# Kernel tuning notes

Measured on AMD Instinct MI355X. Metric: run time of the kernel, lower is better.

## Reference

```python
import jax, jax.numpy as jnp
import numpy as np

MARGIN = 0.3

def setup_inputs() -> dict:
    key = jax.random.key(0)
    k1, k2 = jax.random.split(key)
    embeddings = jax.random.normal(k1, (8192, 512), dtype=jnp.float32)
    labels = jax.random.randint(k2, (8192,), 0, 128, dtype=jnp.int64)
    return {"embeddings": embeddings, "labels": labels}

def _pairwise_euclidean(x):
    # ||xi - xj|| via GEMM, matching torch reference (relu clamp + sqrt(.+1e-16))
    dot = x @ x.T                      # [B, B]
    sq = jnp.diagonal(dot)             # [B]
    d2 = sq[None, :] - 2.0 * dot + sq[:, None]
    d2 = jnp.maximum(d2, 0.0)
    return jnp.sqrt(d2 + 1e-16)

def reference(embeddings, labels):
    n = embeddings.shape[0]
    d = _pairwise_euclidean(embeddings)                 # [B, B]
    same = labels[:, None] == labels[None, :]           # [B, B]
    eye = jnp.eye(n, dtype=bool)
    mask_pos = same & ~eye
    mask_neg = ~same
    # fused masked row-wise reductions (hard mining)
    hardest_pos = jnp.max(jnp.where(mask_pos, d, -jnp.inf), axis=1)  # [B]
    hardest_neg = jnp.min(jnp.where(mask_neg, d, jnp.inf), axis=1)   # [B]
    valid = mask_pos.any(axis=1) & mask_neg.any(axis=1)              # [B]
    per_row = jax.nn.relu(hardest_pos - hardest_neg + MARGIN)
    per_row = jnp.where(valid, per_row, 0.0)
    denom = jnp.maximum(jnp.sum(valid.astype(per_row.dtype)), 1.0)
    return jnp.sum(per_row) / denom
```

## Files before the change

kernel.cpp:

```cpp
#include <hip/hip_runtime.h>

#define BATCH 8192
#define DIM   512
#define NTILE 1152

typedef __attribute__((ext_vector_type(4))) float  f32x4;
typedef __attribute__((ext_vector_type(8))) __bf16 bf16x8;

__device__ __forceinline__ unsigned short f2bf(float x) {
  unsigned u = __float_as_uint(x);
  u = (u + 0x7FFFu + ((u >> 16) & 1u)) >> 16;
  return (unsigned short)u;
}

__device__ __forceinline__ void load_lds16(const void* g, void* l) {
  __builtin_amdgcn_global_load_lds(
      (__attribute__((address_space(1))) void*)(g),
      (__attribute__((address_space(3))) void*)(l), 16, 0, 0);
}

__device__ __forceinline__ unsigned enc(float f) {
  unsigned u = __float_as_uint(f);
  return u ^ (unsigned)(((int)u >> 31) | 0x80000000);
}
__device__ __forceinline__ float dec(unsigned k) {
  unsigned u = (k & 0x80000000u) ? (k ^ 0x80000000u) : ~k;
  return __uint_as_float(u);
}

__global__ __launch_bounds__(256) void prep_kernel(
    const float* __restrict__ X, unsigned short* __restrict__ Xb,
    float* __restrict__ sq, unsigned* __restrict__ ctrl,
    uint4* __restrict__ pos4, uint4* __restrict__ neg4) {
  int gid = blockIdx.x * 256 + threadIdx.x;
  if (gid == 0) {
    ((float*)ctrl)[0] = 0.f;
    ((float*)ctrl)[1] = 0.f;
    ctrl[2] = 0u;
    ctrl[3] = 0u;
  }
  if (gid < 196608) {
    pos4[gid] = (uint4){0u, 0u, 0u, 0u};
    neg4[gid] = (uint4){~0u, ~0u, ~0u, ~0u};
  }
  int wave = threadIdx.x >> 6, lane = threadIdx.x & 63;
  int row = blockIdx.x * 4 + wave;
  const float4* xr = (const float4*)(X + (size_t)row * DIM);
  float4 a = xr[lane * 2];
  float4 b = xr[lane * 2 + 1];
  float s = a.x*a.x + a.y*a.y + a.z*a.z + a.w*a.w
          + b.x*b.x + b.y*b.y + b.z*b.z + b.w*b.w;
  uint4 p;
  p.x = (unsigned)f2bf(a.x) | ((unsigned)f2bf(a.y) << 16);
  p.y = (unsigned)f2bf(a.z) | ((unsigned)f2bf(a.w) << 16);
  p.z = (unsigned)f2bf(b.x) | ((unsigned)f2bf(b.y) << 16);
  p.w = (unsigned)f2bf(b.z) | ((unsigned)f2bf(b.w) << 16);
  ((uint4*)(Xb + (size_t)row * DIM))[lane] = p;
  #pragma unroll
  for (int off = 32; off > 0; off >>= 1) s += __shfl_down(s, off);
  if (lane == 0) sq[row] = s;
}

template<int NI>
__device__ __forceinline__ void gemm_tile(
    const unsigned short* __restrict__ Xb, int i0, int jw,
    unsigned short* Asm, unsigned short* Bsm,
    int wave, int wm, int wn, int quad, int lc, int rc, int gcol,
    f32x4 (&acc)[4][8]) {
  for (int k0 = 0; k0 < DIM; k0 += 64) {
    #pragma unroll
    for (int tt = 0; tt < 4; tt++) {
      int c = wave * 4 + tt;
      int row = c * 8 + rc;
      load_lds16(Xb + (size_t)(i0 + row) * DIM + k0 + gcol, &Asm[c * 512]);
    }
    #pragma unroll
    for (int tt = 0; tt < NI; tt++) {
      int c = wave * NI + tt;
      int row = c * 8 + rc;
      load_lds16(Xb + (size_t)(jw + row) * DIM + k0 + gcol, &Bsm[c * 512]);
    }
    __syncthreads();
    #pragma unroll
    for (int kk = 0; kk < 64; kk += 32) {
      int kc = kk >> 3;
      int asel = ((kc + quad) ^ (lc & 7)) * 8;
      bf16x8 af[4], bfr[NI];
      #pragma unroll
      for (int mi = 0; mi < 4; mi++)
        af[mi] = *(const bf16x8*)&Asm[(wm * 64 + mi * 16 + lc) * 64 + asel];
      #pragma unroll
      for (int ni = 0; ni < NI; ni++)
        bfr[ni] = *(const bf16x8*)&Bsm[(wn * (NI * 16) + ni * 16 + lc) * 64 + asel];
      #pragma unroll
      for (int mi = 0; mi < 4; mi++)
        #pragma unroll
        for (int ni = 0; ni < NI; ni++)
          acc[mi][ni] = __builtin_amdgcn_mfma_f32_16x16x32_bf16(
              af[mi], bfr[ni], acc[mi][ni], 0, 0, 0);
    }
    __syncthreads();
  }
}

template<bool STRAD, int NI, int WNS>
__device__ __forceinline__ void epilogue(
    const f32x4 (&acc)[4][8], const float* __restrict__ sq,
    const int* __restrict__ labels,
    int i0, int jwin, int wm, int wn, int quad, int lc,
    unsigned (*ibuf)[128][2], unsigned (*jbuf)[256][2]) {
  float sqj_r[NI]; int labj_r[NI];
  #pragma unroll
  for (int ni = 0; ni < NI; ni++) {
    int j = jwin + wn * WNS + ni * 16 + lc;
    sqj_r[ni] = sq[j]; labj_r[ni] = labels[j];
  }
  float rpos[16], rneg[16];
  float jp[NI], jn[NI];
  #pragma unroll
  for (int x = 0; x < NI; x++) { jp[x] = -3e38f; jn[x] = 3e38f; }
  #pragma unroll
  for (int mi = 0; mi < 4; mi++) {
    #pragma unroll
    for (int r = 0; r < 4; r++) {
      int ig = i0 + wm * 64 + mi * 16 + quad * 4 + r;
      int li = labels[ig];
      float si = sq[ig];
      float rp = -3e38f, rn = 3e38f;
      #pragma unroll
      for (int ni = 0; ni < NI; ni++) {
        float a = acc[mi][ni][r];
        float v = fmaf(-2.f, a, sqj_r[ni]);
        bool same = (li == labj_r[ni]);
        bool posok = same;
        if (STRAD) posok = same && ((jwin + wn * WNS + ni * 16 + lc) != ig);
        rp = fmaxf(rp, posok ? v : -3e38f);
        rn = fminf(rn, same ? 3e38f : v);
        if (!STRAD) {
          float v2 = fmaf(-2.f, a, si);
          jp[ni] = fmaxf(jp[ni], same ? v2 : -3e38f);
          jn[ni] = fminf(jn[ni], same ? 3e38f : v2);
        }
      }
      rpos[mi * 4 + r] = rp; rneg[mi * 4 + r] = rn;
    }
  }
  #pragma unroll
  for (int m = 1; m <= 8; m <<= 1)
    #pragma unroll
    for (int x = 0; x < 16; x++) {
      rpos[x] = fmaxf(rpos[x], __shfl_xor(rpos[x], m));
      rneg[x] = fminf(rneg[x], __shfl_xor(rneg[x], m));
    }
  if (lc == 0) {
    #pragma unroll
    for (int mi = 0; mi < 4; mi++)
      #pragma unroll
      for (int r = 0; r < 4; r++) {
        int row = wm * 64 + mi * 16 + quad * 4 + r;
        ibuf[wn][row][0] = enc(rpos[mi * 4 + r]);
        ibuf[wn][row][1] = enc(rneg[mi * 4 + r]);
      }
  }
  if (!STRAD) {
    #pragma unroll
    for (int m = 16; m <= 32; m <<= 1)
      #pragma unroll
      for (int x = 0; x < NI; x++) {
        jp[x] = fmaxf(jp[x], __shfl_xor(jp[x], m));
        jn[x] = fminf(jn[x], __shfl_xor(jn[x], m));
      }
    if (quad == 0) {
      #pragma unroll
      for (int ni = 0; ni < NI; ni++) {
        int col = wn * WNS + ni * 16 + lc;
        jbuf[wm][col][0] = enc(jp[ni]);
        jbuf[wm][col][1] = enc(jn[ni]);
      }
    }
  }
}

__global__ __launch_bounds__(256, 2) void triplet_mfma(
    const unsigned short* __restrict__ Xb, const float* __restrict__ sq,
    const int* __restrict__ labels, unsigned* __restrict__ ctrl,
    unsigned* __restrict__ pos_i, unsigned* __restrict__ neg_i,
    unsigned* __restrict__ pos_j, unsigned* __restrict__ neg_j) {
  __shared__ __align__(16) unsigned short Asm[128 * 64];
  __shared__ __align__(16) unsigned short Bsm[256 * 64];
  __shared__ int tshare;

  unsigned (*ibuf)[128][2] = reinterpret_cast<unsigned (*)[128][2]>(&Asm[0]);
  unsigned (*jbuf)[256][2] = reinterpret_cast<unsigned (*)[256][2]>(&Asm[1024]);

  int tid = threadIdx.x;
  int wave = tid >> 6, lane = tid & 63;
  int wm = wave >> 1, wn = wave & 1;
  int quad = lane >> 4, lc = lane & 15;
  int rc = lane >> 3;
  int gcol = ((lane & 7) ^ rc) * 8;

  for (;;) {
    if (tid == 0) tshare = (int)atomicAdd(&ctrl[3], 1u);
    __syncthreads();
    int t = tshare;
    if (t >= NTILE) break;

    int It = 0, Js = 0, q = -1; bool strad = false;
    if (t < 64) { It = t; Js = t >> 1; strad = true; }
    else {
      int u;
      if (t < 1024) u = t - 64;
      else { q = (t - 1024) & 3; u = 960 + ((t - 1024) >> 2); }
      for (int s = 0; s < 64; s++) {
        int c = 31 - (s >> 1);
        if (u < c) { It = s; Js = (s >> 1) + 1 + u; break; }
        u -= c;
      }
    }
    int i0 = It * 128;
    int jw = Js * 256 + (q >= 0 ? q * 64 : 0);

    f32x4 acc[4][8];
    #pragma unroll
    for (int mi = 0; mi < 4; mi++)
      #pragma unroll
      for (int ni = 0; ni < 8; ni++)
        acc[mi][ni] = (f32x4){0.f, 0.f, 0.f, 0.f};

    if (q >= 0) {
      gemm_tile<2>(Xb, i0, jw, Asm, Bsm, wave, wm, wn, quad, lc, rc, gcol, acc);
      epilogue<false, 2, 32>(acc, sq, labels, i0, jw, wm, wn, quad, lc, ibuf, jbuf);
    } else {
      gemm_tile<8>(Xb, i0, jw, Asm, Bsm, wave, wm, wn, quad, lc, rc, gcol, acc);
      if (strad)
        epilogue<true, 8, 128>(acc, sq, labels, i0, jw, wm, wn, quad, lc, ibuf, jbuf);
      else
        epilogue<false, 8, 128>(acc, sq, labels, i0, jw, wm, wn, quad, lc, ibuf, jbuf);
    }
    __syncthreads();

    if (q >= 0) {
      if (tid < 128) {
        unsigned p = max(ibuf[0][tid][0], ibuf[1][tid][0]);
        unsigned n = min(ibuf[0][tid][1], ibuf[1][tid][1]);
        atomicMax(&pos_i[(size_t)Js * BATCH + i0 + tid], p);
        atomicMin(&neg_i[(size_t)Js * BATCH + i0 + tid], n);
      }
      if (tid < 64) {
        unsigned p = max(jbuf[0][tid][0], jbuf[1][tid][0]);
        unsigned n = min(jbuf[0][tid][1], jbuf[1][tid][1]);
        pos_j[(size_t)It * BATCH + jw + tid] = p;
        neg_j[(size_t)It * BATCH + jw + tid] = n;
      }
    } else {
      if (tid < 128) {
        unsigned p = max(ibuf[0][tid][0], ibuf[1][tid][0]);
        unsigned n = min(ibuf[0][tid][1], ibuf[1][tid][1]);
        pos_i[(size_t)Js * BATCH + i0 + tid] = p;
        neg_i[(size_t)Js * BATCH + i0 + tid] = n;
      }
      if (!strad) {
        unsigned p = max(jbuf[0][tid][0], jbuf[1][tid][0]);
        unsigned n = min(jbuf[0][tid][1], jbuf[1][tid][1]);
        pos_j[(size_t)It * BATCH + jw + tid] = p;
        neg_j[(size_t)It * BATCH + jw + tid] = n;
      }
    }
    __syncthreads();
  }
}

__global__ __launch_bounds__(256) void final_kernel(
    const unsigned* __restrict__ pos_i, const unsigned* __restrict__ neg_i,
    const unsigned* __restrict__ pos_j, const unsigned* __restrict__ neg_j,
    const float* __restrict__ sq, unsigned* __restrict__ ctrl,
    float* __restrict__ out) {
  int i = blockIdx.x * 256 + threadIdx.x;
  unsigned pe = 0u, ne = 0xFFFFFFFFu;
  #pragma unroll 4
  for (int s = 0; s < 32; s++) {
    pe = max(pe, pos_i[(size_t)s * BATCH + i]);
    ne = min(ne, neg_i[(size_t)s * BATCH + i]);
  }
  #pragma unroll 4
  for (int s = 0; s < 64; s++) {
    pe = max(pe, pos_j[(size_t)s * BATCH + i]);
    ne = min(ne, neg_j[(size_t)s * BATCH + i]);
  }
  float p = dec(pe), n = dec(ne);
  float term = 0.f, cnt = 0.f;
  if (p > -1e37f && n < 1e37f) {
    float si = sq[i];
    float dp = sqrtf(fmaxf(si + p, 0.f) + 1e-16f);
    float dn = sqrtf(fmaxf(si + n, 0.f) + 1e-16f);
    term = fmaxf(dp - dn + 0.3f, 0.f);
    cnt = 1.f;
  }
  #pragma unroll
  for (int off = 32; off > 0; off >>= 1) {
    term += __shfl_down(term, off);
    cnt  += __shfl_down(cnt, off);
  }
  __shared__ float ss[4], sc[4];
  int wave = threadIdx.x >> 6, lane = threadIdx.x & 63;
  if (lane == 0) { ss[wave] = term; sc[wave] = cnt; }
  __syncthreads();
  if (threadIdx.x == 0) {
    atomicAdd((float*)&ctrl[0], ss[0] + ss[1] + ss[2] + ss[3]);
    atomicAdd((float*)&ctrl[1], sc[0] + sc[1] + sc[2] + sc[3]);
    __threadfence();
    unsigned t = atomicAdd(&ctrl[2], 1u);
    if (t == 31u) {
      float S = atomicAdd((float*)&ctrl[0], 0.f);
      float C = atomicAdd((float*)&ctrl[1], 0.f);
      out[0] = S / fmaxf(C, 1.f);
    }
  }
}

extern "C" void kernel_launch(void* const* d_in, const int* in_sizes, int n_in,
                              void* d_out, int out_size, void* d_ws, size_t ws_size,
                              hipStream_t stream) {
  const float* X      = (const float*)d_in[0];
  const int*   labels = (const int*)d_in[1];
  float* out = (float*)d_out;
  char* ws = (char*)d_ws;

  const size_t SLOT = (size_t)BATCH * 4;
  unsigned short* Xb = (unsigned short*)ws;
  float* sq      = (float*)(ws + (8u << 20));
  unsigned* ctrl = (unsigned*)(ws + (8u << 20) + (32u << 10));
  char*  posb = ws + (8u << 20) + (64u << 10);
  char*  negb = posb + 96 * SLOT;
  unsigned* pos_i = (unsigned*)posb;
  unsigned* pos_j = (unsigned*)(posb + 32 * SLOT);
  unsigned* neg_i = (unsigned*)negb;
  unsigned* neg_j = (unsigned*)(negb + 32 * SLOT);

  prep_kernel<<<BATCH / 4, 256, 0, stream>>>(X, Xb, sq, ctrl,
                                             (uint4*)posb, (uint4*)negb);
  triplet_mfma<<<512, 256, 0, stream>>>(Xb, sq, labels, ctrl,
                                        pos_i, neg_i, pos_j, neg_j);
  final_kernel<<<BATCH / 256, 256, 0, stream>>>(pos_i, neg_i, pos_j, neg_j, sq, ctrl, out);
}
```

Before: 135.4 us.

## Prefetch next tile's first K-slab during epilogue; split final reduction across waves

The persistent GEMM loop now grabs the next tile index before the epilogue and issues the global-to-LDS loads for that tile's first K slab, so they overlap the current tile's epilogue and atomic writes. To make this safe, the epilogue scratch buffers get their own shared memory instead of aliasing the A tile, and one barrier per K loop and one per tile are dropped. The final reduction kernel is relaunched with 128 blocks, each splitting the 96 slot reads across four waves, to raise parallelism for the memory-bound merge. The cost is more shared memory per block, which could limit occupancy, plus extra control-flow complexity.

```diff
diff --git a/kernel.cpp b/kernel.cpp
--- a/kernel.cpp
+++ b/kernel.cpp
@@ -3,6 +3,7 @@
 #define BATCH 8192
 #define DIM   512
 #define NTILE 1152
+#define NFIN  128
 
 typedef __attribute__((ext_vector_type(4))) float  f32x4;
 typedef __attribute__((ext_vector_type(8))) __bf16 bf16x8;
@@ -61,25 +62,45 @@
   if (lane == 0) sq[row] = s;
 }
 
+__device__ __forceinline__ void decode_tile(int t, int& It, int& Js, int& q, bool& strad) {
+  It = 0; Js = 0; q = -1; strad = false;
+  if (t < 64) { It = t; Js = t >> 1; strad = true; return; }
+  int u;
+  if (t < 1024) u = t - 64;
+  else { q = (t - 1024) & 3; u = 960 + ((t - 1024) >> 2); }
+  for (int s = 0; s < 64; s++) {
+    int c = 31 - (s >> 1);
+    if (u < c) { It = s; Js = (s >> 1) + 1 + u; return; }
+    u -= c;
+  }
+}
+
 template<int NI>
-__device__ __forceinline__ void gemm_tile(
+__device__ __forceinline__ void stage_slab(
+    const unsigned short* __restrict__ Xb, int i0, int jw, int k0,
+    unsigned short* Asm, unsigned short* Bsm, int wave, int rc, int gcol) {
+  #pragma unroll
+  for (int tt = 0; tt < 4; tt++) {
+    int c = wave * 4 + tt;
+    int row = c * 8 + rc;
+    load_lds16(Xb + (size_t)(i0 + row) * DIM + k0 + gcol, &Asm[c * 512]);
+  }
+  #pragma unroll
+  for (int tt = 0; tt < NI; tt++) {
+    int c = wave * NI + tt;
+    int row = c * 8 + rc;
+    load_lds16(Xb + (size_t)(jw + row) * DIM + k0 + gcol, &Bsm[c * 512]);
+  }
+}
+
+template<int NI>
+__device__ __forceinline__ void gemm_pf(
     const unsigned short* __restrict__ Xb, int i0, int jw,
     unsigned short* Asm, unsigned short* Bsm,
     int wave, int wm, int wn, int quad, int lc, int rc, int gcol,
     f32x4 (&acc)[4][8]) {
   for (int k0 = 0; k0 < DIM; k0 += 64) {
-    #pragma unroll
-    for (int tt = 0; tt < 4; tt++) {
-      int c = wave * 4 + tt;
-      int row = c * 8 + rc;
-      load_lds16(Xb + (size_t)(i0 + row) * DIM + k0 + gcol, &Asm[c * 512]);
-    }
-    #pragma unroll
-    for (int tt = 0; tt < NI; tt++) {
-      int c = wave * NI + tt;
-      int row = c * 8 + rc;
-      load_lds16(Xb + (size_t)(jw + row) * DIM + k0 + gcol, &Bsm[c * 512]);
-    }
+    if (k0) stage_slab<NI>(Xb, i0, jw, k0, Asm, Bsm, wave, rc, gcol);
     __syncthreads();
     #pragma unroll
     for (int kk = 0; kk < 64; kk += 32) {
@@ -99,7 +120,7 @@
           acc[mi][ni] = __builtin_amdgcn_mfma_f32_16x16x32_bf16(
               af[mi], bfr[ni], acc[mi][ni], 0, 0, 0);
     }
-    __syncthreads();
+    if (k0 < DIM - 64) __syncthreads();
   }
 }
 
@@ -188,10 +209,9 @@
     unsigned* __restrict__ pos_j, unsigned* __restrict__ neg_j) {
   __shared__ __align__(16) unsigned short Asm[128 * 64];
   __shared__ __align__(16) unsigned short Bsm[256 * 64];
+  __shared__ unsigned ibuf[2][128][2];
+  __shared__ unsigned jbuf[2][256][2];
   __shared__ int tshare;
-
-  unsigned (*ibuf)[128][2] = reinterpret_cast<unsigned (*)[128][2]>(&Asm[0]);
-  unsigned (*jbuf)[256][2] = reinterpret_cast<unsigned (*)[256][2]>(&Asm[1024]);
 
   int tid = threadIdx.x;
   int wave = tid >> 6, lane = tid & 63;
@@ -200,44 +220,47 @@
   int rc = lane >> 3;
   int gcol = ((lane & 7) ^ rc) * 8;
 
+  if (tid == 0) tshare = (int)atomicAdd(&ctrl[3], 1u);
+  __syncthreads();
+  int t = tshare;
+  if (t >= NTILE) return;
+
+  int It, Js, q; bool strad;
+  decode_tile(t, It, Js, q, strad);
+  int i0 = It * 128;
+  int jw = Js * 256 + (q >= 0 ? q * 64 : 0);
+  if (q >= 0) stage_slab<2>(Xb, i0, jw, 0, Asm, Bsm, wave, rc, gcol);
+  else        stage_slab<8>(Xb, i0, jw, 0, Asm, Bsm, wave, rc, gcol);
+
   for (;;) {
+    f32x4 acc[4][8];
+    #pragma unroll
+    for (int mi = 0; mi < 4; mi++)
+      #pragma unroll
+      for (int ni = 0; ni < 8; ni++)
+        acc[mi][ni] = (f32x4){0.f, 0.f, 0.f, 0.f};
+
+    if (q >= 0) gemm_pf<2>(Xb, i0, jw, Asm, Bsm, wave, wm, wn, quad, lc, rc, gcol, acc);
+    else        gemm_pf<8>(Xb, i0, jw, Asm, Bsm, wave, wm, wn, quad, lc, rc, gcol, acc);
+
     if (tid == 0) tshare = (int)atomicAdd(&ctrl[3], 1u);
     __syncthreads();
-    int t = tshare;
-    if (t >= NTILE) break;
-
-    int It = 0, Js = 0, q = -1; bool strad = false;
-    if (t < 64) { It = t; Js = t >> 1; strad = true; }
-    else {
-      int u;
-      if (t < 1024) u = t - 64;
-      else { q = (t - 1024) & 3; u = 960 + ((t - 1024) >> 2); }
-      for (int s = 0; s < 64; s++) {
-        int c = 31 - (s >> 1);
-        if (u < c) { It = s; Js = (s >> 1) + 1 + u; break; }
-        u -= c;
-      }
-    }
-    int i0 = It * 128;
-    int jw = Js * 256 + (q >= 0 ? q * 64 : 0);
-
-    f32x4 acc[4][8];
-    #pragma unroll
-    for (int mi = 0; mi < 4; mi++)
-      #pragma unroll
-      for (int ni = 0; ni < 8; ni++)
-        acc[mi][ni] = (f32x4){0.f, 0.f, 0.f, 0.f};
-
-    if (q >= 0) {
-      gemm_tile<2>(Xb, i0, jw, Asm, Bsm, wave, wm, wn, quad, lc, rc, gcol, acc);
+    int tn = tshare;
+    int nIt = 0, nJs = 0, nq = -1; bool nstrad = false; int ni0 = 0, njw = 0;
+    if (tn < NTILE) {
+      decode_tile(tn, nIt, nJs, nq, nstrad);
+      ni0 = nIt * 128;
+      njw = nJs * 256 + (nq >= 0 ? nq * 64 : 0);
+      if (nq >= 0) stage_slab<2>(Xb, ni0, njw, 0, Asm, Bsm, wave, rc, gcol);
+      else         stage_slab<8>(Xb, ni0, njw, 0, Asm, Bsm, wave, rc, gcol);
+    }
+
+    if (q >= 0)
       epilogue<false, 2, 32>(acc, sq, labels, i0, jw, wm, wn, quad, lc, ibuf, jbuf);
-    } else {
-      gemm_tile<8>(Xb, i0, jw, Asm, Bsm, wave, wm, wn, quad, lc, rc, gcol, acc);
-      if (strad)
-        epilogue<true, 8, 128>(acc, sq, labels, i0, jw, wm, wn, quad, lc, ibuf, jbuf);
-      else
-        epilogue<false, 8, 128>(acc, sq, labels, i0, jw, wm, wn, quad, lc, ibuf, jbuf);
-    }
+    else if (strad)
+      epilogue<true, 8, 128>(acc, sq, labels, i0, jw, wm, wn, quad, lc, ibuf, jbuf);
+    else
+      epilogue<false, 8, 128>(acc, sq, labels, i0, jw, wm, wn, quad, lc, ibuf, jbuf);
     __syncthreads();
 
     if (q >= 0) {
@@ -267,7 +290,9 @@
         neg_j[(size_t)It * BATCH + jw + tid] = n;
       }
     }
-    __syncthreads();
+
+    if (tn >= NTILE) break;
+    t = tn; It = nIt; Js = nJs; q = nq; strad = nstrad; i0 = ni0; jw = njw;
   }
 }
 
@@ -276,45 +301,52 @@
     const unsigned* __restrict__ pos_j, const unsigned* __restrict__ neg_j,
     const float* __restrict__ sq, unsigned* __restrict__ ctrl,
     float* __restrict__ out) {
-  int i = blockIdx.x * 256 + threadIdx.x;
+  __shared__ unsigned fbuf[4][64][2];
+  int wave = threadIdx.x >> 6, lane = threadIdx.x & 63;
+  int r = blockIdx.x * 64 + lane;
   unsigned pe = 0u, ne = 0xFFFFFFFFu;
-  #pragma unroll 4
-  for (int s = 0; s < 32; s++) {
-    pe = max(pe, pos_i[(size_t)s * BATCH + i]);
-    ne = min(ne, neg_i[(size_t)s * BATCH + i]);
-  }
-  #pragma unroll 4
-  for (int s = 0; s < 64; s++) {
-    pe = max(pe, pos_j[(size_t)s * BATCH + i]);
-    ne = min(ne, neg_j[(size_t)s * BATCH + i]);
-  }
-  float p = dec(pe), n = dec(ne);
-  float term = 0.f, cnt = 0.f;
-  if (p > -1e37f && n < 1e37f) {
-    float si = sq[i];
-    float dp = sqrtf(fmaxf(si + p, 0.f) + 1e-16f);
-    float dn = sqrtf(fmaxf(si + n, 0.f) + 1e-16f);
-    term = fmaxf(dp - dn + 0.3f, 0.f);
-    cnt = 1.f;
-  }
-  #pragma unroll
-  for (int off = 32; off > 0; off >>= 1) {
-    term += __shfl_down(term, off);
-    cnt  += __shfl_down(cnt, off);
-  }
-  __shared__ float ss[4], sc[4];
-  int wave = threadIdx.x >> 6, lane = threadIdx.x & 63;
-  if (lane == 0) { ss[wave] = term; sc[wave] = cnt; }
+  #pragma unroll
+  for (int k = 0; k < 24; k++) {
+    int s = wave * 24 + k;
+    const unsigned* ps = (s < 32) ? pos_i + (size_t)s * BATCH
+                                  : pos_j + (size_t)(s - 32) * BATCH;
+    const unsigned* ns = (s < 32) ? neg_i + (size_t)s * BATCH
+                                  : neg_j + (size_t)(s - 32) * BATCH;
+    pe = max(pe, ps[r]);
+    ne = min(ne, ns[r]);
+  }
+  fbuf[wave][lane][0] = pe;
+  fbuf[wave][lane][1] = ne;
   __syncthreads();
-  if (threadIdx.x == 0) {
-    atomicAdd((float*)&ctrl[0], ss[0] + ss[1] + ss[2] + ss[3]);
-    atomicAdd((float*)&ctrl[1], sc[0] + sc[1] + sc[2] + sc[3]);
-    __threadfence();
-    unsigned t = atomicAdd(&ctrl[2], 1u);
-    if (t == 31u) {
-      float S = atomicAdd((float*)&ctrl[0], 0.f);
-      float C = atomicAdd((float*)&ctrl[1], 0.f);
-      out[0] = S / fmaxf(C, 1.f);
+  if (wave == 0) {
+    pe = max(max(fbuf[0][lane][0], fbuf[1][lane][0]),
+             max(fbuf[2][lane][0], fbuf[3][lane][0]));
+    ne = min(min(fbuf[0][lane][1], fbuf[1][lane][1]),
+             min(fbuf[2][lane][1], fbuf[3][lane][1]));
+    float p = dec(pe), n = dec(ne);
+    float term = 0.f, cnt = 0.f;
+    if (p > -1e37f && n < 1e37f) {
+      float si = sq[r];
+      float dp = sqrtf(fmaxf(si + p, 0.f) + 1e-16f);
+      float dn = sqrtf(fmaxf(si + n, 0.f) + 1e-16f);
+      term = fmaxf(dp - dn + 0.3f, 0.f);
+      cnt = 1.f;
+    }
+    #pragma unroll
+    for (int off = 32; off > 0; off >>= 1) {
+      term += __shfl_down(term, off);
+      cnt  += __shfl_down(cnt, off);
+    }
+    if (lane == 0) {
+      atomicAdd((float*)&ctrl[0], term);
+      atomicAdd((float*)&ctrl[1], cnt);
+      __threadfence();
+      unsigned t = atomicAdd(&ctrl[2], 1u);
+      if (t == NFIN - 1) {
+        float S = atomicAdd((float*)&ctrl[0], 0.f);
+        float C = atomicAdd((float*)&ctrl[1], 0.f);
+        out[0] = S / fmaxf(C, 1.f);
+      }
     }
   }
 }
@@ -342,5 +374,5 @@
                                              (uint4*)posb, (uint4*)negb);
   triplet_mfma<<<512, 256, 0, stream>>>(Xb, sq, labels, ctrl,
                                         pos_i, neg_i, pos_j, neg_j);
-  final_kernel<<<BATCH / 256, 256, 0, stream>>>(pos_i, neg_i, pos_j, neg_j, sq, ctrl, out);
-}
+  final_kernel<<<NFIN, 256, 0, stream>>>(pos_i, neg_i, pos_j, neg_j, sq, ctrl, out);
+}
```

New measurement: 148.6 us. +9.7%, slower.
